# Kernel tuning notes

Hardware: AMD Instinct MI355X
Metric: run time of the kernel (lower is better)

## Reference

```python
import jax, jax.numpy as jnp
import numpy as np

N_CHEM = 200000
N_GENE = 20000
N_EDGES = 1000000
IN, HID, OUT = 128, 256, 128


def _seg_mean(msg, dst, num_segments):
    # DGL fn.mean: mean of incoming messages; nodes with zero in-degree get 0.
    s = jax.ops.segment_sum(msg, dst, num_segments=num_segments)
    cnt = jax.ops.segment_sum(jnp.ones((msg.shape[0],), msg.dtype), dst,
                              num_segments=num_segments)[:, None]
    return jnp.where(cnt > 0, s / jnp.maximum(cnt, 1.0), 0.0)


def setup_inputs() -> dict:
    key = jax.random.key(0)
    ks = jax.random.split(key, 12)
    d = {
        'src_cg': jax.random.randint(ks[0], (N_EDGES,), 0, N_CHEM, dtype=jnp.int32),
        'dst_cg': jax.random.randint(ks[1], (N_EDGES,), 0, N_GENE, dtype=jnp.int32),
        'src_gc': jax.random.randint(ks[2], (N_EDGES,), 0, N_GENE, dtype=jnp.int32),
        'dst_gc': jax.random.randint(ks[3], (N_EDGES,), 0, N_CHEM, dtype=jnp.int32),
        'embed_chem': jax.random.normal(ks[4], (N_CHEM, IN), jnp.float32) * 0.1,
        'embed_gene': jax.random.normal(ks[5], (N_GENE, IN), jnp.float32) * 0.1,
        'W1_cg': jax.random.normal(ks[6], (IN, HID), jnp.float32) * (1.0 / np.sqrt(IN)),
        'b1_cg': jnp.zeros((HID,), jnp.float32),
        'W1_gc': jax.random.normal(ks[7], (IN, HID), jnp.float32) * (1.0 / np.sqrt(IN)),
        'b1_gc': jnp.zeros((HID,), jnp.float32),
        'W2_cg': jax.random.normal(ks[8], (HID, OUT), jnp.float32) * (1.0 / np.sqrt(HID)),
        'b2_cg': jnp.zeros((OUT,), jnp.float32),
        'W2_gc': jax.random.normal(ks[9], (HID, OUT), jnp.float32) * (1.0 / np.sqrt(HID)),
        'b2_gc': jnp.zeros((OUT,), jnp.float32),
    }
    return d


def _layer(h_chem, h_gene, W_cg, b_cg, W_gc, b_gc, src_cg, dst_cg, src_gc, dst_gc):
    # per-etype linear transform on source features
    Wh_cg = h_chem @ W_cg + b_cg   # [N_CHEM, D]
    Wh_gc = h_gene @ W_gc + b_gc   # [N_GENE, D]
    # copy_u + mean per etype; multi_update_all('sum') -> single etype per dst here
    new_gene = _seg_mean(Wh_cg[src_cg], dst_cg, N_GENE)
    new_chem = _seg_mean(Wh_gc[src_gc], dst_gc, N_CHEM)
    return new_chem, new_gene


def reference(src_cg, dst_cg, src_gc, dst_gc, embed_chem, embed_gene,
              W1_cg, b1_cg, W1_gc, b1_gc, W2_cg, b2_cg, W2_gc, b2_gc):
    h_chem, h_gene = _layer(embed_chem, embed_gene, W1_cg, b1_cg, W1_gc, b1_gc,
                            src_cg, dst_cg, src_gc, dst_gc)
    h_chem = jax.nn.leaky_relu(h_chem, negative_slope=0.01)
    h_gene = jax.nn.leaky_relu(h_gene, negative_slope=0.01)
    h_chem, _ = _layer(h_chem, h_gene, W2_cg, b2_cg, W2_gc, b2_gc,
                       src_cg, dst_cg, src_gc, dst_gc)
    return h_chem  # [N_CHEM, OUT]
```

## Files before the change

### kernel.cpp

```cpp
#include <hip/hip_runtime.h>
#include <stdint.h>
#include <stddef.h>

#define N_CHEM 200000
#define N_GENE 20000
#define N_EDGES 1000000
#define IN_D 128
#define HID_D 256
#define OUT_D 128
#define N_SEG (N_GENE + N_CHEM)

#define NGB 313
#define NCB 391
#define NB  (NGB + NCB)
#define EPB 4096
#define NBA ((2 * N_EDGES + EPB - 1) / EPB)
#define CAP 8192
#define DROPPED 0x80000000

typedef float nfloat4 __attribute__((ext_vector_type(4)));
typedef __attribute__((ext_vector_type(8))) short bf16x8;
typedef __attribute__((ext_vector_type(4))) float f32x4;

__device__ inline unsigned bf16rne(float x) {
    unsigned u = __float_as_uint(x);
    return (u + 0x7FFFu + ((u >> 16) & 1u)) >> 16;
}

__device__ inline int bucket_of(int slot) {
    return (slot < N_GENE) ? (slot >> 6) : (NGB + ((slot - N_GENE) >> 9));
}
__device__ inline int bucket_slot0(int b) {
    return (b < NGB) ? (b << 6) : (N_GENE + ((b - NGB) << 9));
}


__global__ __launch_bounds__(256) void place_convert_kernel(
        const int* __restrict__ src_cg, const int* __restrict__ dst_cg,
        const int* __restrict__ src_gc, const int* __restrict__ dst_gc,
        int* __restrict__ bcur, unsigned* __restrict__ records,
        const float* __restrict__ conv_in, unsigned short* __restrict__ conv_out) {
    if ((int)blockIdx.x >= NBA) {
        int cb = blockIdx.x - NBA;
        const int tid = threadIdx.x;
        #pragma unroll
        for (int q = 0; q < 4; ++q) {
            int i = cb * 1024 + q * 256 + tid;
            if (i < N_CHEM * IN_D / 4) {
                float4 v = *(const float4*)&conv_in[(size_t)i * 4];
                uint2 w;
                w.x = bf16rne(v.x) | (bf16rne(v.y) << 16);
                w.y = bf16rne(v.z) | (bf16rne(v.w) << 16);
                *(uint2*)&conv_out[(size_t)i * 4] = w;
            }
        }
        return;
    }
    __shared__ unsigned stage_rec[EPB];
    __shared__ unsigned short stage_bkt[EPB];
    __shared__ int hist[NB];
    __shared__ int cursor[NB];
    __shared__ int tsum[256];
    const int tid = threadIdx.x;
    const int e0 = blockIdx.x * EPB;
    const int cnt_blk = min(EPB, 2 * N_EDGES - e0);

    for (int i = tid; i < NB; i += 256) hist[i] = 0;
    __syncthreads();

    int slotR[EPB / 256], srcR[EPB / 256];
    #pragma unroll
    for (int q = 0; q < EPB / 256; ++q) {
        int e = e0 + q * 256 + tid;
        int slot = -1, s = 0;
        if (e < N_EDGES)            { slot = dst_cg[e];                    s = src_cg[e]; }
        else if (e < 2 * N_EDGES)   { slot = N_GENE + dst_gc[e - N_EDGES]; s = src_gc[e - N_EDGES]; }
        slotR[q] = slot; srcR[q] = s;
        if (slot >= 0) atomicAdd(&hist[bucket_of(slot)], 1);
    }
    __syncthreads();

    const int b3 = tid * 3;
    int h0 = (b3     < NB) ? hist[b3]     : 0;
    int h1 = (b3 + 1 < NB) ? hist[b3 + 1] : 0;
    int h2 = (b3 + 2 < NB) ? hist[b3 + 2] : 0;
    int ts = h0 + h1 + h2;
    tsum[tid] = ts;
    __syncthreads();
    for (int off = 1; off < 256; off <<= 1) {
        int t = (tid >= off) ? tsum[tid - off] : 0;
        __syncthreads();
        tsum[tid] += t;
        __syncthreads();
    }
    int base = tsum[tid] - ts;
    if (b3     < NB) cursor[b3]     = base;
    if (b3 + 1 < NB) cursor[b3 + 1] = base + h0;
    if (b3 + 2 < NB) cursor[b3 + 2] = base + h0 + h1;
    __syncthreads();

    #pragma unroll
    for (int q = 0; q < EPB / 256; ++q) {
        int slot = slotR[q];
        if (slot >= 0) {
            int b = bucket_of(slot);
            int p = atomicAdd(&cursor[b], 1);
            stage_rec[p] = ((unsigned)(slot - bucket_slot0(b)) << 18) | (unsigned)srcR[q];
            stage_bkt[p] = (unsigned short)b;
        }
    }
    __syncthreads();

    for (int i = tid; i < NB; i += 256) {
        int n = hist[i];
        if (n) {
            int got = atomicAdd(&bcur[i], n);
            int excl_i = cursor[i] - n;
            hist[i] = (got + n <= CAP) ? (i * CAP + got - excl_i) : (int)DROPPED;
        }
    }
    __syncthreads();

    for (int i = tid; i < cnt_blk; i += 256) {
        int d = hist[stage_bkt[i]];
        if (d != (int)DROPPED) records[i + d] = stage_rec[i];
    }
}


__global__ __launch_bounds__(256) void bin_b_kernel(
        const unsigned* __restrict__ records, const int* __restrict__ bcur,
        int* __restrict__ istart, int* __restrict__ iend, int* __restrict__ esrc) {
    __shared__ int hist[512];
    __shared__ int tsum[256];
    const int tid = threadIdx.x;
    const int b = blockIdx.x;
    int slot0 = bucket_slot0(b);
    int nslots = (b < NGB) ? min(64, N_GENE - slot0) : min(512, N_SEG - slot0);
    const int rbase = b * CAP;
    const int E = min(bcur[b], CAP);
    const unsigned* rec = &records[(size_t)b * CAP];

    hist[tid] = 0; hist[tid + 256] = 0;
    __syncthreads();
    for (int i = tid; i < E; i += 256)
        atomicAdd(&hist[rec[i] >> 18], 1);
    __syncthreads();

    int h0 = hist[2 * tid], h1 = hist[2 * tid + 1];
    int ts = h0 + h1;
    tsum[tid] = ts;
    __syncthreads();
    for (int off = 1; off < 256; off <<= 1) {
        int t = (tid >= off) ? tsum[tid - off] : 0;
        __syncthreads();
        tsum[tid] += t;
        __syncthreads();
    }
    int ex = tsum[tid] - ts;
    __syncthreads();
    hist[2 * tid]     = ex;
    hist[2 * tid + 1] = ex + h0;
    if (2 * tid < nslots) {
        istart[slot0 + 2 * tid] = rbase + ex;
        iend[slot0 + 2 * tid]   = rbase + ex + h0;
    }
    if (2 * tid + 1 < nslots) {
        istart[slot0 + 2 * tid + 1] = rbase + ex + h0;
        iend[slot0 + 2 * tid + 1]   = rbase + ex + h0 + h1;
    }
    __syncthreads();

    for (int i = tid; i < E; i += 256) {
        unsigned r = rec[i];
        int p = atomicAdd(&hist[r >> 18], 1);
        esrc[rbase + p] = (int)(r & 0x3FFFFu);
    }
}


__device__ inline void acc_u(float* a, uint4 v) {
    a[0] += __uint_as_float(v.x << 16); a[1] += __uint_as_float(v.x & 0xffff0000u);
    a[2] += __uint_as_float(v.y << 16); a[3] += __uint_as_float(v.y & 0xffff0000u);
    a[4] += __uint_as_float(v.z << 16); a[5] += __uint_as_float(v.z & 0xffff0000u);
    a[6] += __uint_as_float(v.w << 16); a[7] += __uint_as_float(v.w & 0xffff0000u);
}


__global__ __launch_bounds__(256) void gather_mean_bf16_split_kernel(
        const unsigned short* __restrict__ table,
        const int* __restrict__ istart, const int* __restrict__ iend,
        const int* __restrict__ esrc,
        unsigned short* __restrict__ outb, int n) {
    int lane = threadIdx.x & 15;
    int half = (threadIdx.x >> 4) & 1;
    int node = blockIdx.x * 8 + (threadIdx.x >> 5);
    if (node >= n) return;
    int s = istart[node], e = iend[node];
    int deg = e - s;
    int mid = s + ((deg + 1) >> 1);
    int j0 = half ? mid : s;
    int j1 = half ? e   : mid;
    int c = lane << 3;
    float acc[8] = {};
    int j = j0;
    for (; j + 8 <= j1; j += 8) {
        int i0 = esrc[j],     i1 = esrc[j + 1], i2 = esrc[j + 2], i3 = esrc[j + 3];
        int i4 = esrc[j + 4], i5 = esrc[j + 5], i6 = esrc[j + 6], i7 = esrc[j + 7];
        uint4 v0 = *(const uint4*)&table[(size_t)i0 * 128 + c];
        uint4 v1 = *(const uint4*)&table[(size_t)i1 * 128 + c];
        uint4 v2 = *(const uint4*)&table[(size_t)i2 * 128 + c];
        uint4 v3 = *(const uint4*)&table[(size_t)i3 * 128 + c];
        uint4 v4 = *(const uint4*)&table[(size_t)i4 * 128 + c];
        uint4 v5 = *(const uint4*)&table[(size_t)i5 * 128 + c];
        uint4 v6 = *(const uint4*)&table[(size_t)i6 * 128 + c];
        uint4 v7 = *(const uint4*)&table[(size_t)i7 * 128 + c];
        acc_u(acc, v0); acc_u(acc, v1); acc_u(acc, v2); acc_u(acc, v3);
        acc_u(acc, v4); acc_u(acc, v5); acc_u(acc, v6); acc_u(acc, v7);
    }
    for (; j + 4 <= j1; j += 4) {
        uint4 v0 = *(const uint4*)&table[(size_t)esrc[j]     * 128 + c];
        uint4 v1 = *(const uint4*)&table[(size_t)esrc[j + 1] * 128 + c];
        uint4 v2 = *(const uint4*)&table[(size_t)esrc[j + 2] * 128 + c];
        uint4 v3 = *(const uint4*)&table[(size_t)esrc[j + 3] * 128 + c];
        acc_u(acc, v0); acc_u(acc, v1); acc_u(acc, v2); acc_u(acc, v3);
    }
    for (; j < j1; ++j) {
        uint4 v = *(const uint4*)&table[(size_t)esrc[j] * 128 + c];
        acc_u(acc, v);
    }
    #pragma unroll
    for (int q = 0; q < 8; ++q) acc[q] += __shfl_xor(acc[q], 16);
    if (half == 0) {
        float inv = (deg > 0) ? 1.f / (float)deg : 0.f;
        #pragma unroll
        for (int q = 0; q < 8; ++q) acc[q] *= inv;
        uint4 w;
        w.x = bf16rne(acc[0]) | (bf16rne(acc[1]) << 16);
        w.y = bf16rne(acc[2]) | (bf16rne(acc[3]) << 16);
        w.z = bf16rne(acc[4]) | (bf16rne(acc[5]) << 16);
        w.w = bf16rne(acc[6]) | (bf16rne(acc[7]) << 16);
        *(uint4*)&outb[(size_t)node * 128 + c] = w;
    }
}


template<bool NT>
__global__ __launch_bounds__(256) void gather_mean_bf16_kernel(
        const unsigned short* __restrict__ table,
        const int* __restrict__ istart, const int* __restrict__ iend,
        const int* __restrict__ esrc,
        float* __restrict__ out, int n) {
    int lane = threadIdx.x & 15;
    int node = blockIdx.x * 16 + (threadIdx.x >> 4);
    if (node >= n) return;
    int s = istart[node], e = iend[node];
    int c = lane << 3;
    float acc[8] = {};
    int j = s;
    for (; j + 4 <= e; j += 4) {
        uint4 v0 = *(const uint4*)&table[(size_t)esrc[j]     * 128 + c];
        uint4 v1 = *(const uint4*)&table[(size_t)esrc[j + 1] * 128 + c];
        uint4 v2 = *(const uint4*)&table[(size_t)esrc[j + 2] * 128 + c];
        uint4 v3 = *(const uint4*)&table[(size_t)esrc[j + 3] * 128 + c];
        acc_u(acc, v0); acc_u(acc, v1); acc_u(acc, v2); acc_u(acc, v3);
    }
    for (; j < e; ++j) {
        uint4 v = *(const uint4*)&table[(size_t)esrc[j] * 128 + c];
        acc_u(acc, v);
    }
    int deg = e - s;
    float inv = (deg > 0) ? 1.f / (float)deg : 0.f;
    #pragma unroll
    for (int q = 0; q < 8; ++q) acc[q] *= inv;
    float* dst = &out[(size_t)node * 128 + c];
    if (NT) {
        nfloat4 a = { acc[0], acc[1], acc[2], acc[3] };
        nfloat4 b = { acc[4], acc[5], acc[6], acc[7] };
        __builtin_nontemporal_store(a, (nfloat4*)dst);
        __builtin_nontemporal_store(b, (nfloat4*)(dst + 4));
    } else {
        *(float4*)dst       = make_float4(acc[0], acc[1], acc[2], acc[3]);
        *(float4*)(dst + 4) = make_float4(acc[4], acc[5], acc[6], acc[7]);
    }
}


__global__ __launch_bounds__(256) void gather_mean_f32_kernel(
        const float* __restrict__ table,
        const int* __restrict__ istart, const int* __restrict__ iend,
        const int* __restrict__ esrc,
        float* __restrict__ out, int n) {
    int lane = threadIdx.x & 31;
    int node = blockIdx.x * 8 + (threadIdx.x >> 5);
    if (node >= n) return;
    int s = istart[node], e = iend[node];
    int c = lane << 2;
    float4 acc = make_float4(0.f, 0.f, 0.f, 0.f);
    int j = s;
    for (; j + 4 <= e; j += 4) {
        int s0 = esrc[j], s1 = esrc[j + 1], s2 = esrc[j + 2], s3 = esrc[j + 3];
        float4 v0 = *(const float4*)&table[(size_t)s0 * 128 + c];
        float4 v1 = *(const float4*)&table[(size_t)s1 * 128 + c];
        float4 v2 = *(const float4*)&table[(size_t)s2 * 128 + c];
        float4 v3 = *(const float4*)&table[(size_t)s3 * 128 + c];
        acc.x += (v0.x + v1.x) + (v2.x + v3.x);
        acc.y += (v0.y + v1.y) + (v2.y + v3.y);
        acc.z += (v0.z + v1.z) + (v2.z + v3.z);
        acc.w += (v0.w + v1.w) + (v2.w + v3.w);
    }
    for (; j < e; ++j) {
        float4 v = *(const float4*)&table[(size_t)esrc[j] * 128 + c];
        acc.x += v.x; acc.y += v.y; acc.z += v.z; acc.w += v.w;
    }
    int deg = e - s;
    float inv = (deg > 0) ? 1.f / (float)deg : 0.f;
    acc.x *= inv; acc.y *= inv; acc.z *= inv; acc.w *= inv;
    *(float4*)&out[(size_t)node * 128 + c] = acc;
}


__global__ __launch_bounds__(256) void gemm_fused_kernel(
        const unsigned short* __restrict__ A,
        const float* __restrict__ W1,
        const float* __restrict__ b1,
        const float* __restrict__ W2,
        const float* __restrict__ b2,
        const int* __restrict__ istart, const int* __restrict__ iend,
        unsigned short* __restrict__ C,
        int M) {
    constexpr int LDK = 136;
    constexpr int LDH = 264;
    __shared__ unsigned short SAB[2 * 64 * LDK];
    __shared__ unsigned short Ht[64 * LDH];
    unsigned short* As = SAB;
    unsigned short* Ws = SAB + 64 * LDK;
    const int tid  = threadIdx.x;
    const int lane = tid & 63;
    const int w    = tid >> 6;
    const int m0   = blockIdx.x * 64;
    const int l15  = lane & 15;
    const int lhi  = lane >> 4;

    #pragma unroll
    for (int it = 0; it < 4; ++it) {
        int idx = it * 256 + tid;
        int row = idx >> 4;
        int c8  = (idx & 15) << 3;
        uint4 v = make_uint4(0u, 0u, 0u, 0u);
        if (m0 + row < M)
            v = *(const uint4*)&A[(size_t)(m0 + row) * IN_D + c8];
        *(uint4*)&As[row * LDK + c8] = v;
    }
    for (int n0c = 0; n0c < HID_D; n0c += 64) {
        __syncthreads();
        #pragma unroll
        for (int it = 0; it < 32; ++it) {
            int i = it * 256 + tid;
            int k = i >> 6;
            int n = i & 63;
            Ws[n * LDK + k] = (unsigned short)bf16rne(W1[(size_t)k * HID_D + n0c + n]);
        }
        __syncthreads();
        f32x4 acc[4] = {};
        #pragma unroll
        for (int kk = 0; kk < 128; kk += 32) {
            bf16x8 a = *(const bf16x8*)&As[(w * 16 + l15) * LDK + kk + lhi * 8];
            #pragma unroll
            for (int nt = 0; nt < 4; ++nt) {
                bf16x8 b = *(const bf16x8*)&Ws[(nt * 16 + l15) * LDK + kk + lhi * 8];
                acc[nt] = __builtin_amdgcn_mfma_f32_16x16x32_bf16(a, b, acc[nt], 0, 0, 0);
            }
        }
        #pragma unroll
        for (int nt = 0; nt < 4; ++nt) {
            int col = n0c + nt * 16 + l15;
            float bz = b1[col];
            #pragma unroll
            for (int r = 0; r < 4; ++r) {
                int row = w * 16 + lhi * 4 + r;
                if (m0 + row < M) {
                    float v = acc[nt][r] + bz;
                    int deg = iend[m0 + row] - istart[m0 + row];
                    v = (deg == 0) ? 0.f : (v > 0.f ? v : 0.01f * v);
                    Ht[row * LDH + col] = (unsigned short)bf16rne(v);
                }
            }
        }
    }
    __syncthreads();

    f32x4 acc2[8] = {};
    for (int kt = 0; kt < HID_D; kt += 128) {
        #pragma unroll
        for (int it = 0; it < 64; ++it) {
            int i = it * 256 + tid;
            int k = i >> 7;
            int n = i & 127;
            SAB[n * LDK + k] = (unsigned short)bf16rne(W2[(size_t)(kt + k) * OUT_D + n]);
        }
        __syncthreads();
        #pragma unroll
        for (int kk = 0; kk < 128; kk += 32) {
            bf16x8 a = *(const bf16x8*)&Ht[(w * 16 + l15) * LDH + kt + kk + lhi * 8];
            #pragma unroll
            for (int nt = 0; nt < 8; ++nt) {
                bf16x8 b = *(const bf16x8*)&SAB[(nt * 16 + l15) * LDK + kk + lhi * 8];
                acc2[nt] = __builtin_amdgcn_mfma_f32_16x16x32_bf16(a, b, acc2[nt], 0, 0, 0);
            }
        }
        __syncthreads();
    }
    #pragma unroll
    for (int nt = 0; nt < 8; ++nt) {
        int col = nt * 16 + l15;
        float bz = b2[col];
        #pragma unroll
        for (int r = 0; r < 4; ++r) {
            int row = m0 + w * 16 + lhi * 4 + r;
            if (row < M) {
                float v = acc2[nt][r] + bz;
                C[(size_t)row * OUT_D + col] = (unsigned short)bf16rne(v);
            }
        }
    }
}


template<int K, int N, bool MASK_LEAKY, bool BF16_OUT>
__global__ __launch_bounds__(256) void gemm_kernel(const float* __restrict__ A,
                                                   const float* __restrict__ W,
                                                   const float* __restrict__ bias,
                                                   const int* __restrict__ istart,
                                                   const int* __restrict__ iend,
                                                   void* __restrict__ Cout, int M) {
    __shared__ float As[64 * 68];
    __shared__ float Ws[64 * 64];
    const int tid = threadIdx.x;
    const int tx = tid & 15, ty = tid >> 4;
    const int m0 = blockIdx.x * 64;
    const int n0 = blockIdx.y * 64;
    const int r0 = ty << 2, c0 = tx << 2;
    float acc[4][4] = {};

    for (int kt = 0; kt < K; kt += 64) {
        #pragma unroll
        for (int q = 0; q < 4; ++q) {
            int idx = tid + q * 256;
            int row = idx >> 4;
            int c4  = (idx & 15) << 2;
            float4 v = make_float4(0.f, 0.f, 0.f, 0.f);
            if (m0 + row < M)
                v = *(const float4*)&A[(size_t)(m0 + row) * K + kt + c4];
            *(float4*)&As[row * 68 + c4] = v;
        }
        #pragma unroll
        for (int q = 0; q < 4; ++q) {
            int idx = tid + q * 256;
            int k   = idx >> 4;
            int c4  = (idx & 15) << 2;
            *(float4*)&Ws[(k << 6) + c4] =
                *(const float4*)&W[(size_t)(kt + k) * N + n0 + c4];
        }
        __syncthreads();

        #pragma unroll 4
        for (int k = 0; k < 64; k += 4) {
            float a[4][4];
            #pragma unroll
            for (int r = 0; r < 4; ++r) {
                float4 v = *(const float4*)&As[(r0 + r) * 68 + k];
                a[r][0] = v.x; a[r][1] = v.y; a[r][2] = v.z; a[r][3] = v.w;
            }
            #pragma unroll
            for (int kk = 0; kk < 4; ++kk) {
                float4 w = *(const float4*)&Ws[((k + kk) << 6) + c0];
                #pragma unroll
                for (int r = 0; r < 4; ++r) {
                    acc[r][0] = fmaf(a[r][kk], w.x, acc[r][0]);
                    acc[r][1] = fmaf(a[r][kk], w.y, acc[r][1]);
                    acc[r][2] = fmaf(a[r][kk], w.z, acc[r][2]);
                    acc[r][3] = fmaf(a[r][kk], w.w, acc[r][3]);
                }
            }
        }
        __syncthreads();
    }

    float4 b = *(const float4*)&bias[n0 + c0];
    #pragma unroll
    for (int r = 0; r < 4; ++r) {
        int row = m0 + r0 + r;
        if (row < M) {
            float4 v;
            v.x = acc[r][0] + b.x; v.y = acc[r][1] + b.y;
            v.z = acc[r][2] + b.z; v.w = acc[r][3] + b.w;
            if (MASK_LEAKY) {
                int deg = iend[row] - istart[row];
                if (deg == 0) {
                    v = make_float4(0.f, 0.f, 0.f, 0.f);
                } else {
                    v.x = v.x > 0.f ? v.x : 0.01f * v.x;
                    v.y = v.y > 0.f ? v.y : 0.01f * v.y;
                    v.z = v.z > 0.f ? v.z : 0.01f * v.z;
                    v.w = v.w > 0.f ? v.w : 0.01f * v.w;
                }
            }
            if (BF16_OUT) {
                uint2 w;
                w.x = bf16rne(v.x) | (bf16rne(v.y) << 16);
                w.y = bf16rne(v.z) | (bf16rne(v.w) << 16);
                *(uint2*)&((unsigned short*)Cout)[(size_t)row * N + n0 + c0] = w;
            } else {
                *(float4*)&((float*)Cout)[(size_t)row * N + n0 + c0] = v;
            }
        }
    }
}


extern "C" void kernel_launch(void* const* d_in, const int* in_sizes, int n_in,
                              void* d_out, int out_size, void* d_ws, size_t ws_size,
                              hipStream_t stream) {
    const int*   src_cg     = (const int*)d_in[0];
    const int*   dst_cg     = (const int*)d_in[1];
    const int*   src_gc     = (const int*)d_in[2];
    const int*   dst_gc     = (const int*)d_in[3];
    const float* embed_chem = (const float*)d_in[4];
    const float* W1_cg = (const float*)d_in[6];
    const float* b1_cg = (const float*)d_in[7];
    const float* W2_gc = (const float*)d_in[12];
    const float* b2_gc = (const float*)d_in[13];
    float* out = (float*)d_out;

    int* ws_i = (int*)d_ws;
    size_t off = 0;
    int* bcur   = ws_i + off; off += NB;
    int* istart = ws_i + off; off += N_SEG;
    int* iend   = ws_i + off; off += N_SEG;
    off = (off + 3) & ~(size_t)3;
    int* esrc   = ws_i + off; off += (size_t)NB * CAP;
    size_t union_off = off;
    unsigned* records = (unsigned*)(ws_i + union_off);
    unsigned short* agg1b = (unsigned short*)(ws_i + union_off);
    float* agg1f   = (float*)(ws_i + union_off);
    float* h_genef = agg1f + (size_t)N_GENE * IN_D;
    size_t union_sz = (size_t)NB * CAP;
    if (union_sz < (size_t)N_GENE * (IN_D + HID_D)) union_sz = (size_t)N_GENE * (IN_D + HID_D);
    off = union_off + union_sz;
    unsigned short* Wh2b = (unsigned short*)(ws_i + off); off += (size_t)N_GENE * OUT_D / 2;
    unsigned short* embedb = (unsigned short*)(ws_i + off);
    size_t off_full = off + (size_t)N_CHEM * IN_D / 2;
    const bool bf16_embed = ws_size >= off_full * sizeof(int);

    (void)hipMemsetAsync(bcur, 0, NB * sizeof(int), stream);

    const int nconv = bf16_embed ? (N_CHEM * IN_D / 4 + 1023) / 1024 : 0;
    place_convert_kernel<<<NBA + nconv, 256, 0, stream>>>(
        src_cg, dst_cg, src_gc, dst_gc, bcur, records, embed_chem, embedb);
    bin_b_kernel<<<NB, 256, 0, stream>>>(records, bcur, istart, iend, esrc);

    if (bf16_embed) {
        gather_mean_bf16_split_kernel<<<(N_GENE + 7) / 8, 256, 0, stream>>>(
            embedb, istart, iend, esrc, agg1b, N_GENE);
        gemm_fused_kernel<<<(N_GENE + 63) / 64, 256, 0, stream>>>(
            agg1b, W1_cg, b1_cg, W2_gc, b2_gc, istart, iend, Wh2b, N_GENE);
    } else {
        gather_mean_f32_kernel<<<(N_GENE + 7) / 8, 256, 0, stream>>>(
            embed_chem, istart, iend, esrc, agg1f, N_GENE);
        {
            dim3 g((N_GENE + 63) / 64, HID_D / 64), blk(256);
            gemm_kernel<IN_D, HID_D, true, false><<<g, blk, 0, stream>>>(
                agg1f, W1_cg, b1_cg, istart, iend, h_genef, N_GENE);
        }
        {
            dim3 g((N_GENE + 63) / 64, OUT_D / 64), blk(256);
            gemm_kernel<HID_D, OUT_D, false, true><<<g, blk, 0, stream>>>(
                h_genef, W2_gc, b2_gc, istart, iend, Wh2b, N_GENE);
        }
    }

    gather_mean_bf16_kernel<true><<<(N_CHEM + 15) / 16, 256, 0, stream>>>(
        Wh2b, istart + N_GENE, iend + N_GENE, esrc, out, N_CHEM);
}
```

Measured before the change: 380.9 us.

## Pre-transpose weights to bf16 once and split fused GEMM into tiled MFMA kernels

Adds extra blocks to the placement kernel that convert W1 and W2 to bf16 and transpose them once into workspace. The single fused two-GEMM kernel, which reconverted the full weights from fp32 inside every block, is replaced by two generic MFMA GEMM launches tiled over both M and N that load the pre-transposed bf16 weights with vector loads. This removes redundant per-block weight conversion and transposition and raises block-level parallelism. In exchange, the hidden activations now make a round trip through global memory and there is one more kernel launch.

```diff
diff --git a/kernel.cpp b/kernel.cpp
--- a/kernel.cpp
+++ b/kernel.cpp
@@ -15,6 +15,8 @@
 #define NB  (NGB + NCB)
 #define EPB 4096
 #define NBA ((2 * N_EDGES + EPB - 1) / EPB)
+#define NCONV 6250
+#define NWT 16
 #define CAP 8192
 #define DROPPED 0x80000000
 
@@ -39,10 +41,42 @@
         const int* __restrict__ src_cg, const int* __restrict__ dst_cg,
         const int* __restrict__ src_gc, const int* __restrict__ dst_gc,
         int* __restrict__ bcur, unsigned* __restrict__ records,
-        const float* __restrict__ conv_in, unsigned short* __restrict__ conv_out) {
-    if ((int)blockIdx.x >= NBA) {
-        int cb = blockIdx.x - NBA;
-        const int tid = threadIdx.x;
+        const float* __restrict__ conv_in, unsigned short* __restrict__ conv_out,
+        const float* __restrict__ W1, const float* __restrict__ W2,
+        unsigned short* __restrict__ W1t, unsigned short* __restrict__ W2t) {
+    __shared__ unsigned stage_rec[EPB];
+    __shared__ unsigned short stage_bkt[EPB];
+    __shared__ int hist[NB];
+    __shared__ int cursor[NB];
+    __shared__ int tsum[256];
+    const int tid = threadIdx.x;
+    const int bid = blockIdx.x;
+
+    if (bid >= NBA + NCONV) {
+        unsigned short* tile = (unsigned short*)stage_rec;
+        int wb = bid - NBA - NCONV;
+        const float* Wsrc; unsigned short* Wdst; int K, N, kt0, n0;
+        if (wb < 8) { Wsrc = W1; Wdst = W1t; K = 128; N = 256;
+                      kt0 = (wb >> 2) * 64; n0 = (wb & 3) * 64; }
+        else        { wb -= 8; Wsrc = W2; Wdst = W2t; K = 256; N = 128;
+                      kt0 = (wb >> 1) * 64; n0 = (wb & 1) * 64; }
+        #pragma unroll
+        for (int it = 0; it < 16; ++it) {
+            int idx = it * 256 + tid;
+            int r = idx >> 6, c = idx & 63;
+            tile[c * 65 + r] = (unsigned short)bf16rne(Wsrc[(size_t)(kt0 + r) * N + n0 + c]);
+        }
+        __syncthreads();
+        #pragma unroll
+        for (int it = 0; it < 16; ++it) {
+            int idx = it * 256 + tid;
+            int r = idx >> 6, c = idx & 63;
+            Wdst[(size_t)(n0 + r) * K + kt0 + c] = tile[r * 65 + c];
+        }
+        return;
+    }
+    if (bid >= NBA) {
+        int cb = bid - NBA;
         #pragma unroll
         for (int q = 0; q < 4; ++q) {
             int i = cb * 1024 + q * 256 + tid;
@@ -56,13 +90,7 @@
         }
         return;
     }
-    __shared__ unsigned stage_rec[EPB];
-    __shared__ unsigned short stage_bkt[EPB];
-    __shared__ int hist[NB];
-    __shared__ int cursor[NB];
-    __shared__ int tsum[256];
-    const int tid = threadIdx.x;
-    const int e0 = blockIdx.x * EPB;
+    const int e0 = bid * EPB;
     const int cnt_blk = min(EPB, 2 * N_EDGES - e0);
 
     for (int i = tid; i < NB; i += 256) hist[i] = 0;
@@ -320,51 +348,50 @@
 }
 
 
-__global__ __launch_bounds__(256) void gemm_fused_kernel(
+template<int K, int N, bool MASK_LEAKY>
+__global__ __launch_bounds__(256) void gemm_mfma_kernel(
         const unsigned short* __restrict__ A,
-        const float* __restrict__ W1,
-        const float* __restrict__ b1,
-        const float* __restrict__ W2,
-        const float* __restrict__ b2,
+        const unsigned short* __restrict__ Wt,
+        const float* __restrict__ bias,
         const int* __restrict__ istart, const int* __restrict__ iend,
         unsigned short* __restrict__ C,
         int M) {
-    constexpr int LDK = 136;
-    constexpr int LDH = 264;
-    __shared__ unsigned short SAB[2 * 64 * LDK];
-    __shared__ unsigned short Ht[64 * LDH];
-    unsigned short* As = SAB;
-    unsigned short* Ws = SAB + 64 * LDK;
+    constexpr int BK  = 128;
+    constexpr int LDK = BK + 8;
+    __shared__ unsigned short As[64 * LDK];
+    __shared__ unsigned short Ws[64 * LDK];
     const int tid  = threadIdx.x;
     const int lane = tid & 63;
     const int w    = tid >> 6;
-    const int m0   = blockIdx.x * 64;
-    const int l15  = lane & 15;
-    const int lhi  = lane >> 4;
-
-    #pragma unroll
-    for (int it = 0; it < 4; ++it) {
-        int idx = it * 256 + tid;
-        int row = idx >> 4;
-        int c8  = (idx & 15) << 3;
-        uint4 v = make_uint4(0u, 0u, 0u, 0u);
-        if (m0 + row < M)
-            v = *(const uint4*)&A[(size_t)(m0 + row) * IN_D + c8];
-        *(uint4*)&As[row * LDK + c8] = v;
-    }
-    for (int n0c = 0; n0c < HID_D; n0c += 64) {
-        __syncthreads();
-        #pragma unroll
-        for (int it = 0; it < 32; ++it) {
-            int i = it * 256 + tid;
-            int k = i >> 6;
-            int n = i & 63;
-            Ws[n * LDK + k] = (unsigned short)bf16rne(W1[(size_t)k * HID_D + n0c + n]);
-        }
-        __syncthreads();
-        f32x4 acc[4] = {};
-        #pragma unroll
-        for (int kk = 0; kk < 128; kk += 32) {
+    const int m0 = blockIdx.x * 64;
+    const int n0 = blockIdx.y * 64;
+    const int l15 = lane & 15;
+    const int lhi = lane >> 4;
+    f32x4 acc[4] = {};
+
+    for (int kt0 = 0; kt0 < K; kt0 += BK) {
+        #pragma unroll
+        for (int it = 0; it < 4; ++it) {
+            int idx = it * 256 + tid;
+            int row = idx >> 4;
+            int c8  = (idx & 15) << 3;
+            uint4 v = make_uint4(0u, 0u, 0u, 0u);
+            if (m0 + row < M)
+                v = *(const uint4*)&A[(size_t)(m0 + row) * K + kt0 + c8];
+            *(uint4*)&As[row * LDK + c8] = v;
+        }
+        #pragma unroll
+        for (int it = 0; it < 4; ++it) {
+            int idx = it * 256 + tid;
+            int nrow = idx >> 4;
+            int c8   = (idx & 15) << 3;
+            uint4 v = *(const uint4*)&Wt[(size_t)(n0 + nrow) * K + kt0 + c8];
+            *(uint4*)&Ws[nrow * LDK + c8] = v;
+        }
+        __syncthreads();
+
+        #pragma unroll
+        for (int kk = 0; kk < BK; kk += 32) {
             bf16x8 a = *(const bf16x8*)&As[(w * 16 + l15) * LDK + kk + lhi * 8];
             #pragma unroll
             for (int nt = 0; nt < 4; ++nt) {
@@ -372,55 +399,23 @@
                 acc[nt] = __builtin_amdgcn_mfma_f32_16x16x32_bf16(a, b, acc[nt], 0, 0, 0);
             }
         }
-        #pragma unroll
-        for (int nt = 0; nt < 4; ++nt) {
-            int col = n0c + nt * 16 + l15;
-            float bz = b1[col];
-            #pragma unroll
-            for (int r = 0; r < 4; ++r) {
-                int row = w * 16 + lhi * 4 + r;
-                if (m0 + row < M) {
-                    float v = acc[nt][r] + bz;
-                    int deg = iend[m0 + row] - istart[m0 + row];
-                    v = (deg == 0) ? 0.f : (v > 0.f ? v : 0.01f * v);
-                    Ht[row * LDH + col] = (unsigned short)bf16rne(v);
-                }
-            }
-        }
-    }
-    __syncthreads();
-
-    f32x4 acc2[8] = {};
-    for (int kt = 0; kt < HID_D; kt += 128) {
-        #pragma unroll
-        for (int it = 0; it < 64; ++it) {
-            int i = it * 256 + tid;
-            int k = i >> 7;
-            int n = i & 127;
-            SAB[n * LDK + k] = (unsigned short)bf16rne(W2[(size_t)(kt + k) * OUT_D + n]);
-        }
-        __syncthreads();
-        #pragma unroll
-        for (int kk = 0; kk < 128; kk += 32) {
-            bf16x8 a = *(const bf16x8*)&Ht[(w * 16 + l15) * LDH + kt + kk + lhi * 8];
-            #pragma unroll
-            for (int nt = 0; nt < 8; ++nt) {
-                bf16x8 b = *(const bf16x8*)&SAB[(nt * 16 + l15) * LDK + kk + lhi * 8];
-                acc2[nt] = __builtin_amdgcn_mfma_f32_16x16x32_bf16(a, b, acc2[nt], 0, 0, 0);
-            }
-        }
-        __syncthreads();
-    }
+        __syncthreads();
+    }
+
     #pragma unroll
-    for (int nt = 0; nt < 8; ++nt) {
-        int col = nt * 16 + l15;
-        float bz = b2[col];
+    for (int nt = 0; nt < 4; ++nt) {
+        int col = n0 + nt * 16 + l15;
+        float bz = bias[col];
         #pragma unroll
         for (int r = 0; r < 4; ++r) {
             int row = m0 + w * 16 + lhi * 4 + r;
             if (row < M) {
-                float v = acc2[nt][r] + bz;
-                C[(size_t)row * OUT_D + col] = (unsigned short)bf16rne(v);
+                float v = acc[nt][r] + bz;
+                if (MASK_LEAKY) {
+                    int deg = iend[row] - istart[row];
+                    v = (deg == 0) ? 0.f : (v > 0.f ? v : 0.01f * v);
+                }
+                C[(size_t)row * N + col] = (unsigned short)bf16rne(v);
             }
         }
     }
@@ -542,29 +537,40 @@
     int* esrc   = ws_i + off; off += (size_t)NB * CAP;
     size_t union_off = off;
     unsigned* records = (unsigned*)(ws_i + union_off);
-    unsigned short* agg1b = (unsigned short*)(ws_i + union_off);
+    unsigned short* agg1b   = (unsigned short*)(ws_i + union_off);
+    unsigned short* h_geneb = agg1b + (size_t)N_GENE * IN_D;
     float* agg1f   = (float*)(ws_i + union_off);
     float* h_genef = agg1f + (size_t)N_GENE * IN_D;
     size_t union_sz = (size_t)NB * CAP;
     if (union_sz < (size_t)N_GENE * (IN_D + HID_D)) union_sz = (size_t)N_GENE * (IN_D + HID_D);
     off = union_off + union_sz;
     unsigned short* Wh2b = (unsigned short*)(ws_i + off); off += (size_t)N_GENE * OUT_D / 2;
-    unsigned short* embedb = (unsigned short*)(ws_i + off);
-    size_t off_full = off + (size_t)N_CHEM * IN_D / 2;
-    const bool bf16_embed = ws_size >= off_full * sizeof(int);
+    unsigned short* embedb = (unsigned short*)(ws_i + off); off += (size_t)N_CHEM * IN_D / 2;
+    unsigned short* W1t = (unsigned short*)(ws_i + off); off += (size_t)HID_D * IN_D / 2;
+    unsigned short* W2t = (unsigned short*)(ws_i + off); off += (size_t)OUT_D * HID_D / 2;
+    const bool bf16_embed = ws_size >= off * sizeof(int);
 
     (void)hipMemsetAsync(bcur, 0, NB * sizeof(int), stream);
 
-    const int nconv = bf16_embed ? (N_CHEM * IN_D / 4 + 1023) / 1024 : 0;
-    place_convert_kernel<<<NBA + nconv, 256, 0, stream>>>(
-        src_cg, dst_cg, src_gc, dst_gc, bcur, records, embed_chem, embedb);
+    const int nextra = bf16_embed ? (NCONV + NWT) : 0;
+    place_convert_kernel<<<NBA + nextra, 256, 0, stream>>>(
+        src_cg, dst_cg, src_gc, dst_gc, bcur, records, embed_chem, embedb,
+        W1_cg, W2_gc, W1t, W2t);
     bin_b_kernel<<<NB, 256, 0, stream>>>(records, bcur, istart, iend, esrc);
 
     if (bf16_embed) {
         gather_mean_bf16_split_kernel<<<(N_GENE + 7) / 8, 256, 0, stream>>>(
             embedb, istart, iend, esrc, agg1b, N_GENE);
-        gemm_fused_kernel<<<(N_GENE + 63) / 64, 256, 0, stream>>>(
-            agg1b, W1_cg, b1_cg, W2_gc, b2_gc, istart, iend, Wh2b, N_GENE);
+        {
+            dim3 g((N_GENE + 63) / 64, HID_D / 64), blk(256);
+            gemm_mfma_kernel<IN_D, HID_D, true><<<g, blk, 0, stream>>>(
+                agg1b, W1t, b1_cg, istart, iend, h_geneb, N_GENE);
+        }
+        {
+            dim3 g((N_GENE + 63) / 64, OUT_D / 64), blk(256);
+            gemm_mfma_kernel<HID_D, OUT_D, false><<<g, blk, 0, stream>>>(
+                h_geneb, W2t, b2_gc, istart, iend, Wh2b, N_GENE);
+        }
     } else {
         gather_mean_f32_kernel<<<(N_GENE + 7) / 8, 256, 0, stream>>>(
             embed_chem, istart, iend, esrc, agg1f, N_GENE);
```

After: 331.3 us. 13.0% less time.
